# Performance work log

Measured on AMD Instinct MI355X. Metric: run time of the kernel, lower is better.

The kernel has to match this reference:

```python
import jax, jax.numpy as jnp
import numpy as np

B, H, W, C = 16, 64, 64, 768
NH, KD = 12, 64           # num_heads, key_dim; C == NH*KD
NUM_AXES = 2              # attn_axes = [[1],[2]] -> heads split into 2 groups
SCALE = float(np.sqrt(KD))


def setup_inputs() -> dict:
    key = jax.random.key(0)
    ks = jax.random.split(key, 8)
    s = 0.02  # init scale for kernels
    return {
        "queries": jax.random.normal(ks[0], (B, H, W, C), dtype=jnp.float32),
        "values": jax.random.normal(ks[1], (B, H, W, C), dtype=jnp.float32),
        "Wq": jax.random.normal(ks[2], (C, NH, KD), dtype=jnp.float32) * s,
        "bq": jnp.zeros((NH, KD), dtype=jnp.float32),
        "Wk": jax.random.normal(ks[3], (C, NH, KD), dtype=jnp.float32) * s,
        "bk": jnp.zeros((NH, KD), dtype=jnp.float32),
        "Wv": jax.random.normal(ks[4], (C, NH, KD), dtype=jnp.float32) * s,
        "bv": jnp.zeros((NH, KD), dtype=jnp.float32),
        "Wo": jax.random.normal(ks[5], (NH, KD, C), dtype=jnp.float32) * s,
        "bo": jnp.zeros((C,), dtype=jnp.float32),
    }


def _attend_axis_h(q, k, v):
    # attention along the H axis (axis 1); q,k,v: [B,H,W,n,d]
    s = jnp.einsum('bxwnd,bhwnd->bwnhx', k, q) / SCALE  # [B,W,n,Hq,Hk]
    s = jax.nn.softmax(s, axis=-1)
    return jnp.einsum('bwnhx,bxwnd->bhwnd', s, v)


def _attend_axis_w(q, k, v):
    # attention along the W axis (axis 2); q,k,v: [B,H,W,n,d]
    s = jnp.einsum('bhynd,bhwnd->bhnwy', k, q) / SCALE  # [B,H,n,Wq,Wk]
    s = jax.nn.softmax(s, axis=-1)
    return jnp.einsum('bhnwy,bhynd->bhwnd', s, v)


def reference(queries, values, Wq, bq, Wk, bk, Wv, bv, Wo, bo):
    # QKV projections: [B,H,W,C] -> [B,H,W,NH,KD]
    q = jnp.einsum('bhwc,cnd->bhwnd', queries, Wq) + bq
    k = jnp.einsum('bhwc,cnd->bhwnd', values, Wk) + bk
    v = jnp.einsum('bhwc,cnd->bhwnd', values, Wv) + bv
    g = NH // NUM_AXES  # heads per axis group
    o0 = _attend_axis_h(q[..., :g, :], k[..., :g, :], v[..., :g, :])
    o1 = _attend_axis_w(q[..., g:, :], k[..., g:, :], v[..., g:, :])
    out = jnp.concatenate([o0, o1], axis=-2)  # [B,H,W,NH,KD]
    return jnp.einsum('bhwnd,ndc->bhwc', out, Wo) + bo
```

## Files before the change

### kernel.cpp

```cpp
#include <hip/hip_runtime.h>

typedef unsigned short u16;
typedef __bf16 bf16x8 __attribute__((ext_vector_type(8)));
typedef float f32x4 __attribute__((ext_vector_type(4)));

union BF8 {
    bf16x8 v;
    __bf16 e[8];
    u16 h[8];
};

typedef __attribute__((address_space(1))) void gvoid;
typedef __attribute__((address_space(3))) void lvoid;

__device__ __forceinline__ u16 f2bf(float f) {
    __bf16 h = (__bf16)f;
    return __builtin_bit_cast(u16, h);
}

__device__ __forceinline__ void gld_lds16(const void* g, void* l) {
    __builtin_amdgcn_global_load_lds((gvoid*)g, (lvoid*)l, 16, 0, 0);
}

__device__ __forceinline__ f32x4 mfma16(bf16x8 a, bf16x8 b, f32x4 c) {
    return __builtin_amdgcn_mfma_f32_16x16x32_bf16(a, b, c, 0, 0, 0);
}

__global__ __launch_bounds__(256) void transpose_cvt(const float* __restrict__ src,
                                                     u16* __restrict__ dst) {
    __shared__ float t[64][65];
    const int c0 = blockIdx.x * 64, r0 = blockIdx.y * 64;
    const int tid = threadIdx.x;
#pragma unroll
    for (int i = 0; i < 16; ++i) {
        int e = tid + 256 * i;
        int rr = e >> 6, cc = e & 63;
        t[rr][cc] = src[(r0 + rr) * 768 + c0 + cc];
    }
    __syncthreads();
#pragma unroll
    for (int i = 0; i < 16; ++i) {
        int e = tid + 256 * i;
        int rr = e >> 6, cc = e & 63;
        dst[(c0 + rr) * 768 + r0 + cc] = f2bf(t[cc][rr]);
    }
}

template <bool A_F32, bool OUT_F32>
__global__ __launch_bounds__(256) void gemm_kernel(const void* __restrict__ Aptr,
                                                   const u16* __restrict__ Bt,
                                                   const float* __restrict__ bias,
                                                   void* __restrict__ Out) {
    constexpr int ASMEM = A_F32 ? 16384 : 8192;
    __shared__ __attribute__((aligned(16))) char smem[ASMEM + 8192];
    float* Asf = (float*)smem;
    u16* Asb = (u16*)smem;
    u16* Bs = (u16*)(smem + ASMEM);

    const int tid = threadIdx.x;
    const int wid = tid >> 6, lane = tid & 63;
    const int quad = lane >> 4, lm = lane & 15;
    const int mbase = (wid >> 1) * 64, nbase = (wid & 1) * 64;
    const long row0 = (long)blockIdx.y * 128;
    const int n0 = blockIdx.x * 128;

    const f32x4 zero = {0.f, 0.f, 0.f, 0.f};
    f32x4 acc[4][4];
#pragma unroll
    for (int mi = 0; mi < 4; ++mi)
#pragma unroll
        for (int ni = 0; ni < 4; ++ni) acc[mi][ni] = zero;

    for (int kt = 0; kt < 24; ++kt) {
        const int k0 = kt * 32;
        if constexpr (A_F32) {
            const float* A = (const float*)Aptr;
#pragma unroll
            for (int i = 0; i < 4; ++i) {
                int chunk = tid + 256 * i;
                int m = chunk >> 3, s = chunk & 7;
                int kc = s ^ (m & 7);
                gld_lds16(A + (row0 + m) * 768 + k0 + kc * 4, Asf + chunk * 4);
            }
        } else {
            const u16* A = (const u16*)Aptr;
#pragma unroll
            for (int i = 0; i < 2; ++i) {
                int chunk = tid + 256 * i;
                int m = chunk >> 2, s = chunk & 3;
                int kc = s ^ ((m >> 1) & 3);
                gld_lds16(A + (row0 + m) * 768 + k0 + kc * 8, Asb + chunk * 8);
            }
        }
#pragma unroll
        for (int i = 0; i < 2; ++i) {
            int chunk = tid + 256 * i;
            int n = chunk >> 2, s = chunk & 3;
            int kc = s ^ ((n >> 1) & 3);
            gld_lds16(Bt + (long)(n0 + n) * 768 + k0 + kc * 8, Bs + chunk * 8);
        }
        __syncthreads();

        bf16x8 af[4], bfr[4];
#pragma unroll
        for (int mi = 0; mi < 4; ++mi) {
            int m = mbase + mi * 16 + lm;
            if constexpr (A_F32) {
                int c0 = m * 8 + ((quad * 2) ^ (m & 7));
                int c1 = m * 8 + ((quad * 2 + 1) ^ (m & 7));
                f32x4 x0 = *(const f32x4*)(Asf + c0 * 4);
                f32x4 x1 = *(const f32x4*)(Asf + c1 * 4);
                BF8 u;
#pragma unroll
                for (int j = 0; j < 4; ++j) {
                    u.e[j] = (__bf16)x0[j];
                    u.e[4 + j] = (__bf16)x1[j];
                }
                af[mi] = u.v;
            } else {
                int c = m * 4 + (quad ^ ((m >> 1) & 3));
                af[mi] = *(const bf16x8*)(Asb + c * 8);
            }
        }
#pragma unroll
        for (int ni = 0; ni < 4; ++ni) {
            int n = nbase + ni * 16 + lm;
            int c = n * 4 + (quad ^ ((n >> 1) & 3));
            bfr[ni] = *(const bf16x8*)(Bs + c * 8);
        }
#pragma unroll
        for (int mi = 0; mi < 4; ++mi)
#pragma unroll
            for (int ni = 0; ni < 4; ++ni)
                acc[mi][ni] = mfma16(af[mi], bfr[ni], acc[mi][ni]);
        __syncthreads();
    }

#pragma unroll
    for (int mi = 0; mi < 4; ++mi) {
        const long row = row0 + mbase + mi * 16 + quad * 4;
#pragma unroll
        for (int ni = 0; ni < 4; ++ni) {
            const int n = n0 + nbase + ni * 16 + lm;
            const float bv = bias[n];
#pragma unroll
            for (int r = 0; r < 4; ++r) {
                float v = acc[mi][ni][r] + bv;
                if constexpr (OUT_F32)
                    ((float*)Out)[(row + r) * 768 + n] = v;
                else
                    ((u16*)Out)[(row + r) * 768 + n] = f2bf(v);
            }
        }
    }
}

__global__ __launch_bounds__(256) void attn_kernel(const u16* __restrict__ q,
                                                   const u16* __restrict__ k,
                                                   const u16* __restrict__ v,
                                                   u16* __restrict__ o) {
    __shared__ __attribute__((aligned(16))) u16 Qs[64 * 64];
    __shared__ __attribute__((aligned(16))) u16 Ks[64 * 64];
    __shared__ __attribute__((aligned(16))) u16 Vs[64 * 64];
    __shared__ __attribute__((aligned(16))) u16 Vt[64 * 72];

    const int cross = blockIdx.x;
    const int b = blockIdx.y;
    const int head = blockIdx.z;
    const bool axis0 = head < 6;
    const int tid = threadIdx.x;
    const int wid = tid >> 6, lane = tid & 63;
    const int quad = lane >> 4, lm = lane & 15;

    const long base = (long)b * 4096 + (axis0 ? cross : cross * 64);
    const int pstride = axis0 ? 64 : 1;
    const int coloff = head * 64;

#pragma unroll
    for (int i = 0; i < 2; ++i) {
        int chunk = tid + 256 * i;
        int p = chunk >> 3, s = chunk & 7;
        int c = s ^ (p & 7);
        long g = (base + (long)p * pstride) * 768 + coloff + c * 8;
        gld_lds16(q + g, Qs + chunk * 8);
        gld_lds16(k + g, Ks + chunk * 8);
        gld_lds16(v + g, Vs + chunk * 8);
    }
    __syncthreads();

#pragma unroll
    for (int i = 0; i < 2; ++i) {
        int chunk = tid + 256 * i;
        int pos = chunk & 63, cc = chunk >> 6;
        int slot = pos * 8 + (cc ^ (pos & 7));
        BF8 vv;
        vv.v = *(const bf16x8*)(Vs + slot * 8);
#pragma unroll
        for (int j = 0; j < 8; ++j) Vt[(cc * 8 + j) * 72 + pos] = vv.h[j];
    }

    const f32x4 zero = {0.f, 0.f, 0.f, 0.f};
    f32x4 s[4];
#pragma unroll
    for (int nt = 0; nt < 4; ++nt) s[nt] = zero;

    bf16x8 qf[2];
#pragma unroll
    for (int kt = 0; kt < 2; ++kt) {
        int row = 16 * wid + lm;
        int slot = row * 8 + ((kt * 4 + quad) ^ (row & 7));
        qf[kt] = *(const bf16x8*)(Qs + slot * 8);
    }
#pragma unroll
    for (int nt = 0; nt < 4; ++nt)
#pragma unroll
        for (int kt = 0; kt < 2; ++kt) {
            int row = nt * 16 + lm;
            int slot = row * 8 + ((kt * 4 + quad) ^ (row & 7));
            bf16x8 kf = *(const bf16x8*)(Ks + slot * 8);
            s[nt] = mfma16(qf[kt], kf, s[nt]);
        }

    float invl[4];
#pragma unroll
    for (int nt = 0; nt < 4; ++nt) s[nt] = s[nt] * 0.125f;
#pragma unroll
    for (int r = 0; r < 4; ++r) {
        float m = fmaxf(fmaxf(s[0][r], s[1][r]), fmaxf(s[2][r], s[3][r]));
#pragma unroll
        for (int d = 1; d < 16; d <<= 1) m = fmaxf(m, __shfl_xor(m, d));
        float l = 0.f;
#pragma unroll
        for (int nt = 0; nt < 4; ++nt) {
            float p = exp2f((s[nt][r] - m) * 1.44269504f);
            s[nt][r] = p;
            l += p;
        }
#pragma unroll
        for (int d = 1; d < 16; d <<= 1) l += __shfl_xor(l, d);
        invl[r] = 1.f / l;
    }

#pragma unroll
    for (int nt = 0; nt < 4; ++nt)
#pragma unroll
        for (int r = 0; r < 4; ++r) {
            int h = 16 * wid + quad * 4 + r;
            int c = nt * 2 + (lm >> 3);
            Qs[(h * 8 + (c ^ (h & 7))) * 8 + (lm & 7)] = f2bf(s[nt][r]);
        }
    __syncthreads();

    f32x4 oacc[4];
#pragma unroll
    for (int nt = 0; nt < 4; ++nt) oacc[nt] = zero;
#pragma unroll
    for (int kt = 0; kt < 2; ++kt) {
        int row = 16 * wid + lm;
        int slot = row * 8 + ((kt * 4 + quad) ^ (row & 7));
        bf16x8 pf = *(const bf16x8*)(Qs + slot * 8);
#pragma unroll
        for (int nt = 0; nt < 4; ++nt) {
            bf16x8 vf = *(const bf16x8*)(Vt + (nt * 16 + lm) * 72 + kt * 32 + quad * 8);
            oacc[nt] = mfma16(pf, vf, oacc[nt]);
        }
    }

#pragma unroll
    for (int nt = 0; nt < 4; ++nt)
#pragma unroll
        for (int r = 0; r < 4; ++r) {
            int p = 16 * wid + quad * 4 + r;
            long grow = base + (long)p * pstride;
            o[grow * 768 + coloff + nt * 16 + lm] = f2bf(oacc[nt][r] * invl[r]);
        }
}

extern "C" void kernel_launch(void* const* d_in, const int* in_sizes, int n_in,
                              void* d_out, int out_size, void* d_ws, size_t ws_size,
                              hipStream_t stream) {
    const float* queries = (const float*)d_in[0];
    const float* values = (const float*)d_in[1];
    const float* Wq = (const float*)d_in[2];
    const float* bq = (const float*)d_in[3];
    const float* Wk = (const float*)d_in[4];
    const float* bk = (const float*)d_in[5];
    const float* Wv = (const float*)d_in[6];
    const float* bv = (const float*)d_in[7];
    const float* Wo = (const float*)d_in[8];
    const float* bo = (const float*)d_in[9];

    const long MAT = 65536L * 768;
    const long WMAT = 768L * 768;
    u16* qws = (u16*)d_ws;
    u16* kws = qws + MAT;
    u16* vws = kws + MAT;
    u16* aws = vws + MAT;
    u16* wtq = aws + MAT;
    u16* wtk = wtq + WMAT;
    u16* wtv = wtk + WMAT;
    u16* wto = wtv + WMAT;

    dim3 tb(256);
    dim3 tg(12, 12);
    transpose_cvt<<<tg, tb, 0, stream>>>(Wq, wtq);
    transpose_cvt<<<tg, tb, 0, stream>>>(Wk, wtk);
    transpose_cvt<<<tg, tb, 0, stream>>>(Wv, wtv);
    transpose_cvt<<<tg, tb, 0, stream>>>(Wo, wto);

    dim3 gg(6, 512);
    gemm_kernel<true, false><<<gg, tb, 0, stream>>>(queries, wtq, bq, qws);
    gemm_kernel<true, false><<<gg, tb, 0, stream>>>(values, wtk, bk, kws);
    gemm_kernel<true, false><<<gg, tb, 0, stream>>>(values, wtv, bv, vws);

    attn_kernel<<<dim3(64, 16, 12), tb, 0, stream>>>(qws, kws, vws, aws);

    gemm_kernel<false, true><<<gg, tb, 0, stream>>>(aws, wto, bo, (float*)d_out);
}
```

Before: 1.139 ms.

## Fuse K and V projections into one launch with XCD-aware block swizzle

Merges the K and V projection GEMMs, which share the same fp32 input, into a single launch of 12 column tiles per row panel. It also remaps the 1D block index so that all column tiles of a row panel land on the same XCD (bid & 7) and run close together in time. The aim is to reuse the fp32 input rows in that XCD's L2 instead of re-reading them from HBM, and to save a launch. The per-block branch that picks between the two weight, bias and output pointers adds a small amount of overhead.

```diff
diff --git a/kernel.cpp b/kernel.cpp
--- a/kernel.cpp
+++ b/kernel.cpp
@@ -46,23 +46,35 @@
     }
 }
 
-template <bool A_F32, bool OUT_F32>
-__global__ __launch_bounds__(256) void gemm_kernel(const void* __restrict__ Aptr,
-                                                   const u16* __restrict__ Bt,
-                                                   const float* __restrict__ bias,
-                                                   void* __restrict__ Out) {
+template <bool A_F32, bool OUT_F32, bool FUSE>
+__global__ __launch_bounds__(256) void gemm_kernel(
+    const void* __restrict__ Aptr,
+    const u16* __restrict__ Bt0, const float* __restrict__ bias0, void* __restrict__ Out0,
+    const u16* __restrict__ Bt1, const float* __restrict__ bias1, void* __restrict__ Out1) {
     constexpr int ASMEM = A_F32 ? 16384 : 8192;
+    constexpr int J = FUSE ? 12 : 6;
     __shared__ __attribute__((aligned(16))) char smem[ASMEM + 8192];
     float* Asf = (float*)smem;
     u16* Asb = (u16*)smem;
     u16* Bs = (u16*)(smem + ASMEM);
 
+    const int bid = blockIdx.x;
+    const int xcd = bid & 7;
+    const int local = bid >> 3;
+    const int j = local % J;
+    const int mp = xcd * 64 + local / J;
+
+    const bool first = !FUSE || (j < 6);
+    const u16* Bt = first ? Bt0 : Bt1;
+    const float* bias = first ? bias0 : bias1;
+    void* Out = first ? Out0 : Out1;
+
     const int tid = threadIdx.x;
     const int wid = tid >> 6, lane = tid & 63;
     const int quad = lane >> 4, lm = lane & 15;
     const int mbase = (wid >> 1) * 64, nbase = (wid & 1) * 64;
-    const long row0 = (long)blockIdx.y * 128;
-    const int n0 = blockIdx.x * 128;
+    const long row0 = (long)mp * 128;
+    const int n0 = (FUSE ? (j % 6) : j) * 128;
 
     const f32x4 zero = {0.f, 0.f, 0.f, 0.f};
     f32x4 acc[4][4];
@@ -112,9 +124,9 @@
                 f32x4 x1 = *(const f32x4*)(Asf + c1 * 4);
                 BF8 u;
 #pragma unroll
-                for (int j = 0; j < 4; ++j) {
-                    u.e[j] = (__bf16)x0[j];
-                    u.e[4 + j] = (__bf16)x1[j];
+                for (int jj = 0; jj < 4; ++jj) {
+                    u.e[jj] = (__bf16)x0[jj];
+                    u.e[4 + jj] = (__bf16)x1[jj];
                 }
                 af[mi] = u.v;
             } else {
@@ -196,7 +208,7 @@
         BF8 vv;
         vv.v = *(const bf16x8*)(Vs + slot * 8);
 #pragma unroll
-        for (int j = 0; j < 8; ++j) Vt[(cc * 8 + j) * 72 + pos] = vv.h[j];
+        for (int jj = 0; jj < 8; ++jj) Vt[(cc * 8 + jj) * 72 + pos] = vv.h[jj];
     }
 
     const f32x4 zero = {0.f, 0.f, 0.f, 0.f};
@@ -308,12 +320,13 @@
     transpose_cvt<<<tg, tb, 0, stream>>>(Wv, wtv);
     transpose_cvt<<<tg, tb, 0, stream>>>(Wo, wto);
 
-    dim3 gg(6, 512);
-    gemm_kernel<true, false><<<gg, tb, 0, stream>>>(queries, wtq, bq, qws);
-    gemm_kernel<true, false><<<gg, tb, 0, stream>>>(values, wtk, bk, kws);
-    gemm_kernel<true, false><<<gg, tb, 0, stream>>>(values, wtv, bv, vws);
+    gemm_kernel<true, false, false><<<dim3(512 * 6), tb, 0, stream>>>(
+        queries, wtq, bq, qws, nullptr, nullptr, nullptr);
+    gemm_kernel<true, false, true><<<dim3(512 * 12), tb, 0, stream>>>(
+        values, wtk, bk, kws, wtv, bv, vws);
 
     attn_kernel<<<dim3(64, 16, 12), tb, 0, stream>>>(qws, kws, vws, aws);
 
-    gemm_kernel<false, true><<<gg, tb, 0, stream>>>(aws, wto, bo, (float*)d_out);
-}
+    gemm_kernel<false, true, false><<<dim3(512 * 6), tb, 0, stream>>>(
+        aws, wto, bo, (float*)d_out, nullptr, nullptr, nullptr);
+}
```

Result: faster. 994.0 us (-12.7%).
